# Performance work log

Hardware: AMD Instinct MI355X
Metric: run time of the kernel (lower is better)

## Reference

```python
import jax, jax.numpy as jnp
import numpy as np

CHANNELS_CHOICE = np.array([8, 16, 24, 32, 40, 48, 56, 64])
MAX_C = 64
B, H, W_SP = 128, 32, 32
N_EDGES = 6
# edge list per intermediate node: (edge_weight_index, source_node_index)
EDGES = [[(0, 0)], [(1, 0), (2, 1)], [(3, 0), (4, 1), (5, 2)]]


def setup_inputs() -> dict:
    key = jax.random.key(0)
    k1, k2, k3, k4 = jax.random.split(key, 4)
    inputs = jax.random.normal(k1, (B, MAX_C, H, W_SP), dtype=jnp.float32)
    alphas1 = jax.random.uniform(k2, (8,), dtype=jnp.float32)  # input-width arch weights
    alphas2 = jax.random.uniform(k3, (8,), dtype=jnp.float32)  # output-width arch weights
    # shared master 3x3 conv weight per edge (OIHW)
    W = jax.random.normal(k4, (N_EDGES, MAX_C, MAX_C, 3, 3), dtype=jnp.float32) * 0.05
    return {"inputs": inputs, "alphas1": alphas1, "alphas2": alphas2, "W": W}


def _channel_scale(alphas1, alphas2, dtype):
    # mask[c, i] = 1 if channel c is inside width choice CHANNELS_CHOICE[i]
    mask = (jnp.arange(MAX_C)[:, None] < jnp.asarray(CHANNELS_CHOICE)[None, :]).astype(dtype)  # [64, 8]
    a_in = mask @ alphas1   # [64] cumulative input-channel weight
    a_out = mask @ alphas2  # [64] cumulative output-channel weight
    return a_out[:, None] * a_in[None, :]  # [64, 64]


def _edge(x, w, scale):
    # weighted-combi of all (c1, c2) channel-sliced sub-convs == one conv with scaled weight
    w_eff = w * scale[:, :, None, None]
    return jax.lax.conv_general_dilated(
        jax.nn.relu(x), w_eff, window_strides=(1, 1), padding="SAME",
        dimension_numbers=("NCHW", "OIHW", "NCHW"))


def reference(inputs, alphas1, alphas2, W):
    scale = _channel_scale(alphas1, alphas2, inputs.dtype)
    nodes = [inputs]
    for node_edges in EDGES:
        feat = 0.0
        for l, src in node_edges:
            feat = feat + _edge(nodes[src], W[l], scale)
        nodes.append(feat)
    return nodes[-1]
```

## Files before the change

kernel.cpp:

```cpp
#include <hip/hip_runtime.h>
#include <hip/hip_bf16.h>


typedef __bf16 bf16x8 __attribute__((ext_vector_type(8)));
typedef float floatx4 __attribute__((ext_vector_type(4)));
typedef unsigned int uint32;

#define PADW 34
#define PIMG (PADW * PADW)
#define ROWB (PADW * 64 * 2)
#define A_LDS (8 * ROWB)
#define B_LDS (3 * 64 * 64 * 2)
#define A_CHUNKS (A_LDS / 16)
#define B_CHUNKS (B_LDS / 16)

__device__ __forceinline__ void gld16(const char* g, char* l) {
    __builtin_amdgcn_global_load_lds(
        (const __attribute__((address_space(1))) uint32*)g,
        (__attribute__((address_space(3))) uint32*)l, 16, 0, 0);
}

__global__ void prep_weights(const float* __restrict__ a1,
                             const float* __restrict__ a2,
                             const float* __restrict__ W,
                             __hip_bfloat16* __restrict__ wt) {
    int idx = blockIdx.x * 256 + threadIdx.x;
    int i = idx & 63;
    int o = (idx >> 6) & 63;
    int rest = idx >> 12;
    int t = rest % 9;
    int l = rest / 9;
    int ji = i >> 3, jo = o >> 3;
    float ain = 0.f, aout = 0.f;
#pragma unroll
    for (int j = 0; j < 8; ++j) {
        ain  += (j >= ji) ? a1[j] : 0.f;
        aout += (j >= jo) ? a2[j] : 0.f;
    }
    float v = W[(size_t)((l * 64 + o) * 64 + i) * 9 + t] * ain * aout;
    size_t e = (size_t)(l * 9 + t) * 4096 + o * 64 +
               ((((i >> 3) ^ (o & 7)) << 3) + (i & 7));
    wt[e] = __float2bfloat16(v);
}

__global__ void relu_pad(const float* __restrict__ in,
                         __hip_bfloat16* __restrict__ r0) {
    __shared__ float tile[32][65];
    int b = blockIdx.x >> 5, y = blockIdx.x & 31;
    int tid = threadIdx.x;
    int x = tid & 31, c0 = tid >> 5;
    const float* ip = in + ((size_t)b * 64 * 32 + y) * 32 + x;
#pragma unroll
    for (int cc = 0; cc < 8; ++cc) {
        int c = cc * 8 + c0;
        tile[x][c] = fmaxf(ip[(size_t)c * 1024], 0.f);
    }
    __syncthreads();
    int o = tid & 63, xg = tid >> 6;
    int p0 = (b * PADW + y + 1) * PADW + 1;
#pragma unroll
    for (int xx = 0; xx < 8; ++xx) {
        int xq = xx * 4 + xg;
        int p = p0 + xq;
        size_t e = (size_t)p * 64 + ((((o >> 3) ^ (p & 7)) << 3) + (o & 7));
        r0[e] = __float2bfloat16(tile[xq][o]);
    }
}

__global__ void zero_halo(__hip_bfloat16* r0, __hip_bfloat16* r1,
                          __hip_bfloat16* r2) {
    int b = blockIdx.x;
    int tid = threadIdx.x;
    __hip_bfloat16* bufs[3] = {r0, r1, r2};
#pragma unroll
    for (int f = 0; f < 3; ++f) {
        uint32* buf = (uint32*)(bufs[f] + (size_t)b * PIMG * 64);
        for (int idx = tid; idx < 132 * 32; idx += 256) {
            int slot = idx >> 5, u = idx & 31;
            int yy, xx;
            if (slot < 34)      { yy = 0;  xx = slot; }
            else if (slot < 68) { yy = 33; xx = slot - 34; }
            else { int s2 = slot - 68; yy = 1 + (s2 >> 1); xx = (s2 & 1) * 33; }
            buf[(size_t)(yy * PADW + xx) * 32 + u] = 0u;
        }
    }
}

template <int NSRC, bool FINAL>
__global__ __launch_bounds__(256) void conv_stage(
    const __hip_bfloat16* __restrict__ s0,
    const __hip_bfloat16* __restrict__ s1,
    const __hip_bfloat16* __restrict__ s2,
    const __hip_bfloat16* __restrict__ wt,
    void* __restrict__ dstv, int l0) {
    __shared__ char smem[A_LDS + B_LDS];
    int tid = threadIdx.x;
    int wv = tid >> 6, lane = tid & 63;
    int quad = lane >> 4, l15 = lane & 15;
    int blk = blockIdx.x;
    int b = blk >> 2, y0 = (blk & 3) << 3;

    const char* srcs[3] = {(const char*)s0, (const char*)s1, (const char*)s2};

    floatx4 acc[4][4];
#pragma unroll
    for (int m = 0; m < 4; ++m)
#pragma unroll
        for (int n = 0; n < 4; ++n) acc[m][n] = (floatx4){0.f, 0.f, 0.f, 0.f};

#pragma unroll
    for (int s = 0; s < NSRC; ++s) {
        const char* gS = srcs[s];
        const char* gW = (const char*)wt + (size_t)(l0 + s) * 9 * 8192;
#pragma unroll
        for (int ky = 0; ky < 3; ++ky) {
            __syncthreads();
            {
                const char* gA = gS + (size_t)(b * PADW + y0 + ky) * PADW * 128;
#pragma unroll
                for (int it = 0; it < 9; ++it) {
                    int c = it * 256 + tid;
                    if (it < 8 || tid < A_CHUNKS - 2048)
                        gld16(gA + (size_t)c * 16,
                              smem + (it * 256 + wv * 64) * 16);
                }
            }
            {
                const char* gB = gW + (size_t)(ky * 3) * 8192;
#pragma unroll
                for (int it = 0; it < 6; ++it) {
                    int c = it * 256 + tid;
                    gld16(gB + (size_t)c * 16,
                          smem + A_LDS + (it * 256 + wv * 64) * 16);
                }
            }
            __syncthreads();

#pragma unroll
            for (int kx = 0; kx < 3; ++kx)
#pragma unroll
                for (int q = 0; q < 2; ++q) {
                    bf16x8 Af[4], Bf[4];
#pragma unroll
                    for (int m = 0; m < 4; ++m) {
                        int arow = 2 * wv + (m >> 1);
                        int apx  = ((m & 1) << 4) + l15 + kx;
                        int ph = (2 * (b * PADW + y0 + arow + ky)) & 7;
                        int slot = ((q << 2) + quad) ^ ((ph + apx) & 7);
                        Af[m] = *(const bf16x8*)(smem + arow * ROWB +
                                                 apx * 128 + slot * 16);
                    }
#pragma unroll
                    for (int n = 0; n < 4; ++n) {
                        int o = (n << 4) + l15;
                        int slot = ((q << 2) + quad) ^ (l15 & 7);
                        Bf[n] = *(const bf16x8*)(smem + A_LDS + kx * 8192 +
                                                 o * 128 + slot * 16);
                    }
#pragma unroll
                    for (int m = 0; m < 4; ++m)
#pragma unroll
                        for (int n = 0; n < 4; ++n)
                            acc[m][n] = __builtin_amdgcn_mfma_f32_16x16x32_bf16(
                                Af[m], Bf[n], acc[m][n], 0, 0, 0);
                }
        }
    }

    if (FINAL) {
        float* out = (float*)dstv;
#pragma unroll
        for (int m = 0; m < 4; ++m) {
            int row = y0 + 2 * wv + (m >> 1);
#pragma unroll
            for (int n = 0; n < 4; ++n) {
                int o = (n << 4) + l15;
#pragma unroll
                for (int r = 0; r < 4; ++r) {
                    int x = ((m & 1) << 4) + (quad << 2) + r;
                    out[(((size_t)b * 64 + o) * 32 + row) * 32 + x] = acc[m][n][r];
                }
            }
        }
    } else {
        __hip_bfloat16* out = (__hip_bfloat16*)dstv;
#pragma unroll
        for (int m = 0; m < 4; ++m) {
            int row = y0 + 2 * wv + (m >> 1);
#pragma unroll
            for (int n = 0; n < 4; ++n) {
                int o = (n << 4) + l15;
#pragma unroll
                for (int r = 0; r < 4; ++r) {
                    int x = ((m & 1) << 4) + (quad << 2) + r;
                    int p = (b * PADW + row + 1) * PADW + x + 1;
                    float v = fmaxf(acc[m][n][r], 0.f);
                    size_t e = (size_t)p * 64 +
                               ((((o >> 3) ^ (p & 7)) << 3) + (o & 7));
                    out[e] = __float2bfloat16(v);
                }
            }
        }
    }
}

extern "C" void kernel_launch(void* const* d_in, const int* in_sizes, int n_in,
                              void* d_out, int out_size, void* d_ws,
                              size_t ws_size, hipStream_t stream) {
    const float* inputs  = (const float*)d_in[0];
    const float* alphas1 = (const float*)d_in[1];
    const float* alphas2 = (const float*)d_in[2];
    const float* W       = (const float*)d_in[3];
    char* ws = (char*)d_ws;

    __hip_bfloat16* wt = (__hip_bfloat16*)(ws);
    __hip_bfloat16* r0 = (__hip_bfloat16*)(ws + ((size_t)1 << 20));
    __hip_bfloat16* r1 = (__hip_bfloat16*)(ws + ((size_t)20 << 20));
    __hip_bfloat16* r2 = (__hip_bfloat16*)(ws + ((size_t)40 << 20));
    float* out = (float*)d_out;

    prep_weights<<<864, 256, 0, stream>>>(alphas1, alphas2, W, wt);
    relu_pad<<<128 * 32, 256, 0, stream>>>(inputs, r0);
    zero_halo<<<128, 256, 0, stream>>>(r0, r1, r2);

    conv_stage<1, false><<<512, 256, 0, stream>>>(r0, r1, r2, wt, (void*)r1, 0);
    conv_stage<2, false><<<512, 256, 0, stream>>>(r0, r1, r2, wt, (void*)r2, 1);
    conv_stage<3, true ><<<512, 256, 0, stream>>>(r0, r1, r2, wt, (void*)out, 3);
}
```

Measured before the change: 159.7 us.

## Stage full input halo once per source and double-buffer per-tap weights

Each conv block now loads the whole 10-row padded input window into LDS once per source image, instead of reloading an 8-row window for every kernel row ky. Weights are streamed one 3x3 tap at a time into two alternating LDS buffers, so the next tap's load is issued while MFMAs run on the current one. This cuts redundant global-to-LDS traffic for the activations by about threefold. In exchange there is a barrier after every tap instead of two per ky, and the input reload between sources is not overlapped with compute.

```diff
diff --git a/kernel.cpp b/kernel.cpp
--- a/kernel.cpp
+++ b/kernel.cpp
@@ -9,10 +9,9 @@
 #define PADW 34
 #define PIMG (PADW * PADW)
 #define ROWB (PADW * 64 * 2)
-#define A_LDS (8 * ROWB)
-#define B_LDS (3 * 64 * 64 * 2)
+#define A_LDS (10 * ROWB)
+#define TAPB (64 * 64 * 2)
 #define A_CHUNKS (A_LDS / 16)
-#define B_CHUNKS (B_LDS / 16)
 
 __device__ __forceinline__ void gld16(const char* g, char* l) {
     __builtin_amdgcn_global_load_lds(
@@ -93,7 +92,7 @@
     const __hip_bfloat16* __restrict__ s2,
     const __hip_bfloat16* __restrict__ wt,
     void* __restrict__ dstv, int l0) {
-    __shared__ char smem[A_LDS + B_LDS];
+    __shared__ char smem[A_LDS + 2 * TAPB];
     int tid = threadIdx.x;
     int wv = tid >> 6, lane = tid & 63;
     int quad = lane >> 4, l15 = lane & 15;
@@ -101,6 +100,25 @@
     int b = blk >> 2, y0 = (blk & 3) << 3;
 
     const char* srcs[3] = {(const char*)s0, (const char*)s1, (const char*)s2};
+    const char* gW = (const char*)wt + (size_t)l0 * 9 * (size_t)TAPB;
+
+    auto stage_A = [&](int s) {
+        const char* gA = srcs[s] + (size_t)(b * PADW + y0) * PADW * 128;
+#pragma unroll
+        for (int it = 0; it < 11; ++it) {
+            int c = it * 256 + tid;
+            if (it < 10 || tid < 160)
+                gld16(gA + (size_t)c * 16, smem + (it * 256 + wv * 64) * 16);
+        }
+    };
+    auto stage_B = [&](int T) {
+        const char* gB = gW + (size_t)T * TAPB;
+        char* dst = smem + A_LDS + (T & 1) * TAPB;
+#pragma unroll
+        for (int it = 0; it < 2; ++it)
+            gld16(gB + (size_t)(it * 256 + tid) * 16,
+                  dst + (it * 256 + wv * 64) * 16);
+    };
 
     floatx4 acc[4][4];
 #pragma unroll
@@ -108,62 +126,48 @@
 #pragma unroll
         for (int n = 0; n < 4; ++n) acc[m][n] = (floatx4){0.f, 0.f, 0.f, 0.f};
 
-#pragma unroll
-    for (int s = 0; s < NSRC; ++s) {
-        const char* gS = srcs[s];
-        const char* gW = (const char*)wt + (size_t)(l0 + s) * 9 * 8192;
-#pragma unroll
-        for (int ky = 0; ky < 3; ++ky) {
+    stage_A(0);
+    stage_B(0);
+    __syncthreads();
+
+#pragma unroll
+    for (int T = 0; T < 9 * NSRC; ++T) {
+        int s = T / 9, tl = T % 9, ky = tl / 3, kx = tl % 3, buf = T & 1;
+        if (T + 1 < 9 * NSRC) stage_B(T + 1);
+
+#pragma unroll
+        for (int q = 0; q < 2; ++q) {
+            bf16x8 Af[4], Bf[4];
+#pragma unroll
+            for (int m = 0; m < 4; ++m) {
+                int arow = 2 * wv + (m >> 1) + ky;
+                int apx  = ((m & 1) << 4) + l15 + kx;
+                int R = b * PADW + y0 + arow;
+                int slot = ((q << 2) + quad) ^ ((2 * R + apx) & 7);
+                Af[m] = *(const bf16x8*)(smem + arow * ROWB +
+                                         apx * 128 + slot * 16);
+            }
+#pragma unroll
+            for (int n = 0; n < 4; ++n) {
+                int o = (n << 4) + l15;
+                int slot = ((q << 2) + quad) ^ (l15 & 7);
+                Bf[n] = *(const bf16x8*)(smem + A_LDS + buf * TAPB +
+                                         o * 128 + slot * 16);
+            }
+#pragma unroll
+            for (int m = 0; m < 4; ++m)
+#pragma unroll
+                for (int n = 0; n < 4; ++n)
+                    acc[m][n] = __builtin_amdgcn_mfma_f32_16x16x32_bf16(
+                        Af[m], Bf[n], acc[m][n], 0, 0, 0);
+        }
+
+        if (T + 1 < 9 * NSRC) {
             __syncthreads();
-            {
-                const char* gA = gS + (size_t)(b * PADW + y0 + ky) * PADW * 128;
-#pragma unroll
-                for (int it = 0; it < 9; ++it) {
-                    int c = it * 256 + tid;
-                    if (it < 8 || tid < A_CHUNKS - 2048)
-                        gld16(gA + (size_t)c * 16,
-                              smem + (it * 256 + wv * 64) * 16);
-                }
-            }
-            {
-                const char* gB = gW + (size_t)(ky * 3) * 8192;
-#pragma unroll
-                for (int it = 0; it < 6; ++it) {
-                    int c = it * 256 + tid;
-                    gld16(gB + (size_t)c * 16,
-                          smem + A_LDS + (it * 256 + wv * 64) * 16);
-                }
-            }
-            __syncthreads();
-
-#pragma unroll
-            for (int kx = 0; kx < 3; ++kx)
-#pragma unroll
-                for (int q = 0; q < 2; ++q) {
-                    bf16x8 Af[4], Bf[4];
-#pragma unroll
-                    for (int m = 0; m < 4; ++m) {
-                        int arow = 2 * wv + (m >> 1);
-                        int apx  = ((m & 1) << 4) + l15 + kx;
-                        int ph = (2 * (b * PADW + y0 + arow + ky)) & 7;
-                        int slot = ((q << 2) + quad) ^ ((ph + apx) & 7);
-                        Af[m] = *(const bf16x8*)(smem + arow * ROWB +
-                                                 apx * 128 + slot * 16);
-                    }
-#pragma unroll
-                    for (int n = 0; n < 4; ++n) {
-                        int o = (n << 4) + l15;
-                        int slot = ((q << 2) + quad) ^ (l15 & 7);
-                        Bf[n] = *(const bf16x8*)(smem + A_LDS + kx * 8192 +
-                                                 o * 128 + slot * 16);
-                    }
-#pragma unroll
-                    for (int m = 0; m < 4; ++m)
-#pragma unroll
-                        for (int n = 0; n < 4; ++n)
-                            acc[m][n] = __builtin_amdgcn_mfma_f32_16x16x32_bf16(
-                                Af[m], Bf[n], acc[m][n], 0, 0, 0);
-                }
+            if (tl == 8) {
+                stage_A(s + 1);
+                __syncthreads();
+            }
         }
     }
 
```

Result: no change. 159.8 us (+0.1%).
